# Kernel tuning notes

Hardware: AMD Instinct MI355X
Metric: run time of the kernel (lower is better)

The kernel has to match this reference:

```python
import jax, jax.numpy as jnp
import numpy as np

N_NODES = 50000
NEG_SLOPE = 0.2


def _gat_layer(x, src, dst, W, att_src, att_dst, bias, concat):
    # x: [N, F_in]; W: [F_in, H*D]; att_*: [H, D]; bias: [H*D] or [D]
    H, D = att_src.shape
    N = x.shape[0]
    h = (x @ W).reshape(N, H, D)                       # [N, H, D]
    a_s = jnp.einsum('nhd,hd->nh', h, att_src)         # [N, H]
    a_d = jnp.einsum('nhd,hd->nh', h, att_dst)
    e = a_s[src] + a_d[dst]                            # [E, H]
    e = jnp.where(e > 0, e, NEG_SLOPE * e)             # LeakyReLU(0.2)
    # segment softmax over incoming edges of each target node
    e_max = jax.ops.segment_max(e, dst, num_segments=N)
    ex = jnp.exp(e - e_max[dst])
    denom = jax.ops.segment_sum(ex, dst, num_segments=N)
    alpha = ex / denom[dst]                            # [E, H]
    msg = h[src] * alpha[:, :, None]                   # [E, H, D]
    out = jax.ops.segment_sum(msg, dst, num_segments=N)  # [N, H, D]
    if concat:
        out = out.reshape(N, H * D)
    else:
        out = out.mean(axis=1)
    return out + bias


def _forward(x, edge_index, W1, att_src1, att_dst1, b1, W2, att_src2, att_dst2, b2):
    N = x.shape[0]
    loop = jnp.arange(N, dtype=edge_index.dtype)
    src = jnp.concatenate([edge_index[0], loop])       # add self-loops (PyG default)
    dst = jnp.concatenate([edge_index[1], loop])
    h = _gat_layer(x, src, dst, W1, att_src1, att_dst1, b1, concat=True)
    h = jax.nn.elu(h)
    h = _gat_layer(h, src, dst, W2, att_src2, att_dst2, b2, concat=False)
    return jax.nn.log_softmax(h, axis=-1)


def setup_inputs() -> dict:
    key = jax.random.key(0)
    ks = jax.random.split(key, 12)
    N, E, F_in, F_out, H, D = N_NODES, 1600000, 128, 64, 8, 32
    glorot = lambda k, shp: jax.random.normal(k, shp, jnp.float32) * np.sqrt(2.0 / (shp[0] + shp[-1]))
    return {
        'x': jax.random.normal(ks[0], (N, F_in), jnp.float32),
        'edge_index': jax.random.randint(ks[1], (2, E), 0, N, jnp.int64),
        'W1': glorot(ks[2], (F_in, H * D)),
        'att_src1': glorot(ks[3], (H, D)),
        'att_dst1': glorot(ks[4], (H, D)),
        'b1': jnp.zeros((H * D,), jnp.float32),
        'W2': glorot(ks[5], (H * D, F_out)),
        'att_src2': glorot(ks[6], (1, F_out)),
        'att_dst2': glorot(ks[7], (1, F_out)),
        'b2': jnp.zeros((F_out,), jnp.float32),
    }


def reference(x, edge_index, W1, att_src1, att_dst1, b1, W2, att_src2, att_dst2, b2):
    return _forward(x, edge_index, W1, att_src1, att_dst1, b1, W2, att_src2, att_dst2, b2)
```

## Files before the change

kernel.cpp:

```cpp
#include <hip/hip_runtime.h>
#include <hip/hip_bf16.h>
#include <math.h>


#define FIN 128
#define C1 256
#define NH 8
#define HD 32
#define C2 64
#define CH1 64

typedef float floatx2 __attribute__((ext_vector_type(2)));
typedef short bf16x8 __attribute__((ext_vector_type(8)));
typedef float f32x4 __attribute__((ext_vector_type(4)));

__device__ __forceinline__ float blo(unsigned u) { return __uint_as_float(u << 16); }
__device__ __forceinline__ float bhi(unsigned u) { return __uint_as_float(u & 0xffff0000u); }
__device__ __forceinline__ unsigned pkbf(float a, float b) {
    unsigned ua = __float_as_uint(a), ub = __float_as_uint(b);
    ua += 0x7fff + ((ua >> 16) & 1);
    ub += 0x7fff + ((ub >> 16) & 1);
    return (ua >> 16) | (ub & 0xffff0000u);
}

__global__ void init_kernel(const float* __restrict__ W1, const float* __restrict__ W2,
                            int* __restrict__ cnt, unsigned short* __restrict__ w1t,
                            unsigned short* __restrict__ w2t, int n) {
    int i = blockIdx.x * 256 + threadIdx.x;
    if (i < n) cnt[i] = 1;
    if (i < C1 * FIN) {
        int j = i >> 7, k = i & 127;
        float v = W1[(size_t)k * C1 + j];
        w1t[i] = (unsigned short)(pkbf(v, v) & 0xffffu);
    } else if (i < C1 * FIN + C2 * C1) {
        int j2 = i - C1 * FIN;
        int j = j2 >> 8, k = j2 & 255;
        float v = W2[(size_t)k * C2 + j];
        w2t[j2] = (unsigned short)(pkbf(v, v) & 0xffffu);
    }
}

__global__ void hist_kernel(const int* __restrict__ ei, int E, int T,
                            int* cnt, int* __restrict__ offs) {
    int base = blockIdx.x * 256 + threadIdx.x;
    if (base >= T) return;
    int d[4], o[4];
    #pragma unroll
    for (int i = 0; i < 4; ++i) {
        int e = base + i * T;
        d[i] = (e < E) ? ei[E + e] : -1;
    }
    #pragma unroll
    for (int i = 0; i < 4; ++i)
        if (d[i] >= 0) o[i] = atomicAdd(&cnt[d[i]], 1);
    #pragma unroll
    for (int i = 0; i < 4; ++i)
        if (d[i] >= 0) offs[base + i * T] = o[i];
}

__global__ void scan1_kernel(const int* __restrict__ cnt, int n,
                             int* __restrict__ pref, int* __restrict__ bsum) {
    int tid = threadIdx.x, lane = tid & 63, w = tid >> 6;
    int i = blockIdx.x * 256 + tid;
    int v = (i < n) ? cnt[i] : 0;
    int sc = v;
    #pragma unroll
    for (int d = 1; d < 64; d <<= 1) {
        int t = __shfl_up(sc, d, 64);
        if (lane >= d) sc += t;
    }
    __shared__ int ws[4];
    if (lane == 63) ws[w] = sc;
    __syncthreads();
    int woff = 0;
    #pragma unroll
    for (int k = 0; k < 4; ++k) woff += (k < w) ? ws[k] : 0;
    if (i < n) pref[i] = woff + sc - v;
    if (tid == 255) bsum[blockIdx.x] = woff + sc;
}

__global__ void scan2_kernel(int* bsum, int nb) {
    int tid = threadIdx.x, lane = tid & 63, w = tid >> 6;
    int v = (tid < nb) ? bsum[tid] : 0;
    int sc = v;
    #pragma unroll
    for (int d = 1; d < 64; d <<= 1) {
        int t = __shfl_up(sc, d, 64);
        if (lane >= d) sc += t;
    }
    __shared__ int ws[4];
    if (lane == 63) ws[w] = sc;
    __syncthreads();
    int woff = 0;
    #pragma unroll
    for (int k = 0; k < 4; ++k) woff += (k < w) ? ws[k] : 0;
    __syncthreads();
    if (tid < nb) bsum[tid] = woff + sc - v;
}

__global__ void scan3_kernel(const int* __restrict__ pref, const int* __restrict__ bsum,
                             int n, int ETOT, int* __restrict__ rowptr,
                             int* __restrict__ colb) {
    int i = blockIdx.x * 256 + threadIdx.x;
    if (i < n) {
        int rp = pref[i] + bsum[blockIdx.x];
        rowptr[i] = rp;
        colb[rp] = i;
    }
    if (i == 0) rowptr[n] = ETOT;
}

__global__ void scatter_kernel(const int* __restrict__ ei, const int* __restrict__ rowptr,
                               const int* __restrict__ offs, int E, int T,
                               int* __restrict__ colb) {
    int base = blockIdx.x * 256 + threadIdx.x;
    if (base >= T) return;
    #pragma unroll
    for (int i = 0; i < 4; ++i) {
        int e = base + i * T;
        if (e >= E) continue;
        int src = ei[e], dst = ei[E + e];
        colb[rowptr[dst] + offs[e]] = src;
    }
}

__global__ __launch_bounds__(256) void gemm1_mfma(
    const float* __restrict__ x, const unsigned short* __restrict__ w1t,
    const float* __restrict__ att_s, const float* __restrict__ att_d,
    unsigned char* __restrict__ h1, float* __restrict__ as1, float* __restrict__ ad1, int Nn) {
    __shared__ __align__(16) unsigned char sA[64 * 256];
    int tid = threadIdx.x;
    int row0 = blockIdx.x * 64;
    #pragma unroll
    for (int rep = 0; rep < 4; ++rep) {
        int flat = rep * 256 + tid;
        int row = flat >> 4, c16 = flat & 15;
        uint4 v = make_uint4(0u, 0u, 0u, 0u);
        if (row0 + row < Nn) {
            const float4* p = reinterpret_cast<const float4*>(
                x + (size_t)(row0 + row) * FIN + c16 * 8);
            float4 f0 = p[0], f1 = p[1];
            v.x = pkbf(f0.x, f0.y); v.y = pkbf(f0.z, f0.w);
            v.z = pkbf(f1.x, f1.y); v.w = pkbf(f1.z, f1.w);
        }
        *reinterpret_cast<uint4*>(sA + ((row * 256 + c16 * 16) ^ ((row & 7) << 4))) = v;
    }
    __syncthreads();
    int w = tid >> 6, l = tid & 63;
    int lr = l & 15, lq = l >> 4;
    int arow = w * 16 + lr;
    bf16x8 a[4];
    #pragma unroll
    for (int ks = 0; ks < 4; ++ks)
        a[ks] = *reinterpret_cast<const bf16x8*>(
            sA + ((arow * 256 + ks * 64 + lq * 16) ^ ((arow & 7) << 4)));
    const unsigned char* wb = reinterpret_cast<const unsigned char*>(w1t);
    float ps[4] = {0.f, 0.f, 0.f, 0.f}, pd[4] = {0.f, 0.f, 0.f, 0.f};
    #pragma unroll
    for (int nt = 0; nt < 16; ++nt) {
        f32x4 acc = {0.f, 0.f, 0.f, 0.f};
        #pragma unroll
        for (int ks = 0; ks < 4; ++ks) {
            bf16x8 b = *reinterpret_cast<const bf16x8*>(
                wb + (size_t)(nt * 16 + lr) * 256 + ks * 64 + lq * 16);
            acc = __builtin_amdgcn_mfma_f32_16x16x32_bf16(a[ks], b, acc, 0, 0, 0);
        }
        int col = nt * 16 + lr;
        float sa = att_s[col], da = att_d[col];
        #pragma unroll
        for (int reg = 0; reg < 4; ++reg) {
            int row = row0 + w * 16 + lq * 4 + reg;
            if (row < Nn) {
                unsigned pk = __builtin_amdgcn_cvt_pk_fp8_f32(acc[reg], acc[reg], 0, false);
                h1[(size_t)row * C1 + col] = (unsigned char)(pk & 0xffu);
            }
            ps[reg] = fmaf(acc[reg], sa, ps[reg]);
            pd[reg] = fmaf(acc[reg], da, pd[reg]);
        }
        if (nt & 1) {
            #pragma unroll
            for (int reg = 0; reg < 4; ++reg) {
                #pragma unroll
                for (int mk = 8; mk >= 1; mk >>= 1) {
                    ps[reg] += __shfl_xor(ps[reg], mk, 64);
                    pd[reg] += __shfl_xor(pd[reg], mk, 64);
                }
            }
            if (lr == 0) {
                int hh = nt >> 1;
                #pragma unroll
                for (int reg = 0; reg < 4; ++reg) {
                    int row = row0 + w * 16 + lq * 4 + reg;
                    if (row < Nn) {
                        as1[row * NH + hh] = ps[reg];
                        ad1[row * NH + hh] = pd[reg];
                    }
                }
            }
            #pragma unroll
            for (int reg = 0; reg < 4; ++reg) { ps[reg] = 0.f; pd[reg] = 0.f; }
        }
    }
}

__global__ __launch_bounds__(128) void agg1_kernel(
    const int* __restrict__ rowptr, const int* __restrict__ colb,
    const float* __restrict__ as1, const float* __restrict__ ad1,
    const unsigned char* __restrict__ h1, const float* __restrict__ b1,
    __hip_bfloat16* __restrict__ x1e, int N) {
    int wid = threadIdx.x >> 6, lane = threadIdx.x & 63;
    int n = blockIdx.x * 2 + wid;
    __shared__ float sp[2][CH1 * 9];
    __shared__ int soff[2][CH1];
    __shared__ float advs[2][NH];
    if (n >= N) return;
    int start = rowptr[n], end = rowptr[n + 1];
    int h = lane >> 3, sub = lane & 7;
    int half = lane >> 5, l5 = lane & 31;
    int hq = l5 >> 2;
    soff[wid][lane] = 0;
    if (lane < NH) advs[wid][lane] = ad1[n * NH + lane];
    float adr[NH];
    #pragma unroll
    for (int hh = 0; hh < NH; ++hh) adr[hh] = advs[wid][hh];

    float m = -INFINITY, denom = 0.f;
    floatx2 A01 = {0.f, 0.f}, A23 = {0.f, 0.f}, A45 = {0.f, 0.f}, A67 = {0.f, 0.f};
    for (int base = start; base < end; base += CH1) {
        int cn = min(CH1, end - base);
        if (lane < cn) {
            int s = colb[base + lane];
            soff[wid][lane] = s << 8;
            const float4* ap = reinterpret_cast<const float4*>(as1 + (size_t)s * NH);
            float4 q0 = ap[0], q1 = ap[1];
            float av[8] = {q0.x, q0.y, q0.z, q0.w, q1.x, q1.y, q1.z, q1.w};
            #pragma unroll
            for (int hh = 0; hh < NH; ++hh) {
                float e = av[hh] + adr[hh];
                e = e > 0.f ? e : 0.2f * e;
                sp[wid][lane * 9 + hh] = e;
            }
        }
        float cmax = -INFINITY;
        for (int e = sub; e < cn; e += 8) cmax = fmaxf(cmax, sp[wid][e * 9 + h]);
        #pragma unroll
        for (int mk = 4; mk >= 1; mk >>= 1) cmax = fmaxf(cmax, __shfl_xor(cmax, mk, 64));
        float newm = fmaxf(m, cmax);
        float scale = __expf(m - newm);
        float scale_g = __shfl(scale, hq << 3, 64);
        floatx2 s2 = {scale_g, scale_g};
        A01 *= s2; A23 *= s2; A45 *= s2; A67 *= s2;
        denom *= scale; m = newm;
        float psum = 0.f;
        for (int e = sub; e < cn; e += 8) {
            float p = __expf(sp[wid][e * 9 + h] - m);
            sp[wid][e * 9 + h] = p;
            psum += p;
        }
        #pragma unroll
        for (int mk = 4; mk >= 1; mk >>= 1) psum += __shfl_xor(psum, mk, 64);
        denom += psum;
        #pragma unroll 2
        for (int e2 = 0; e2 < cn; e2 += 2) {
            int e = e2 + half;
            bool ok = e < cn;
            int off = soff[wid][ok ? e : 0];
            float p = ok ? sp[wid][e * 9 + hq] : 0.f;
            floatx2 p2 = {p, p};
            uint2 u = *reinterpret_cast<const uint2*>(h1 + off + l5 * 8);
            floatx2 f01 = __builtin_amdgcn_cvt_pk_f32_fp8((int)u.x, false);
            floatx2 f23 = __builtin_amdgcn_cvt_pk_f32_fp8((int)u.x, true);
            floatx2 f45 = __builtin_amdgcn_cvt_pk_f32_fp8((int)u.y, false);
            floatx2 f67 = __builtin_amdgcn_cvt_pk_f32_fp8((int)u.y, true);
            A01 = __builtin_elementwise_fma(p2, f01, A01);
            A23 = __builtin_elementwise_fma(p2, f23, A23);
            A45 = __builtin_elementwise_fma(p2, f45, A45);
            A67 = __builtin_elementwise_fma(p2, f67, A67);
        }
    }
    float a0 = A01.x, a1 = A01.y, a2 = A23.x, a3 = A23.y;
    float a4 = A45.x, a5 = A45.y, a6 = A67.x, a7 = A67.y;
    a0 += __shfl_xor(a0, 32, 64); a1 += __shfl_xor(a1, 32, 64);
    a2 += __shfl_xor(a2, 32, 64); a3 += __shfl_xor(a3, 32, 64);
    a4 += __shfl_xor(a4, 32, 64); a5 += __shfl_xor(a5, 32, 64);
    a6 += __shfl_xor(a6, 32, 64); a7 += __shfl_xor(a7, 32, 64);
    float invd = 1.f / __shfl(denom, hq << 3, 64);
    if (half == 0) {
        const float4* bp = reinterpret_cast<const float4*>(b1 + l5 * 8);
        float4 bv0 = bp[0], bv1 = bp[1];
        float v0 = a0 * invd + bv0.x, v1 = a1 * invd + bv0.y;
        float v2 = a2 * invd + bv0.z, v3 = a3 * invd + bv0.w;
        float v4 = a4 * invd + bv1.x, v5 = a5 * invd + bv1.y;
        float v6 = a6 * invd + bv1.z, v7 = a7 * invd + bv1.w;
        v0 = v0 > 0.f ? v0 : __expf(v0) - 1.f;
        v1 = v1 > 0.f ? v1 : __expf(v1) - 1.f;
        v2 = v2 > 0.f ? v2 : __expf(v2) - 1.f;
        v3 = v3 > 0.f ? v3 : __expf(v3) - 1.f;
        v4 = v4 > 0.f ? v4 : __expf(v4) - 1.f;
        v5 = v5 > 0.f ? v5 : __expf(v5) - 1.f;
        v6 = v6 > 0.f ? v6 : __expf(v6) - 1.f;
        v7 = v7 > 0.f ? v7 : __expf(v7) - 1.f;
        uint4 w;
        w.x = pkbf(v0, v1); w.y = pkbf(v2, v3);
        w.z = pkbf(v4, v5); w.w = pkbf(v6, v7);
        *reinterpret_cast<uint4*>(x1e + (size_t)n * C1 + l5 * 8) = w;
    }
}

__global__ __launch_bounds__(256) void gemm2_mfma(
    const unsigned short* __restrict__ x1e, const unsigned short* __restrict__ w2t,
    const float* __restrict__ att_s2, const float* __restrict__ att_d2,
    unsigned char* __restrict__ h2, float* __restrict__ as2, float* __restrict__ ad2, int Nn) {
    __shared__ __align__(16) unsigned char sA[64 * 512];
    int tid = threadIdx.x;
    int row0 = blockIdx.x * 64;
    #pragma unroll
    for (int rep = 0; rep < 8; ++rep) {
        int flat = rep * 256 + tid;
        int row = flat >> 5, c16 = flat & 31;
        uint4 v = make_uint4(0u, 0u, 0u, 0u);
        if (row0 + row < Nn)
            v = *reinterpret_cast<const uint4*>(
                reinterpret_cast<const unsigned char*>(x1e) + (size_t)(row0 + row) * 512 + c16 * 16);
        *reinterpret_cast<uint4*>(sA + ((row * 512 + c16 * 16) ^ ((row & 7) << 4))) = v;
    }
    __syncthreads();
    int w = tid >> 6, l = tid & 63;
    int lr = l & 15, lq = l >> 4;
    int arow = w * 16 + lr;
    bf16x8 a[8];
    #pragma unroll
    for (int ks = 0; ks < 8; ++ks)
        a[ks] = *reinterpret_cast<const bf16x8*>(
            sA + ((arow * 512 + ks * 64 + lq * 16) ^ ((arow & 7) << 4)));
    const unsigned char* wb = reinterpret_cast<const unsigned char*>(w2t);
    float ps[4] = {0.f, 0.f, 0.f, 0.f}, pd[4] = {0.f, 0.f, 0.f, 0.f};
    #pragma unroll
    for (int nt = 0; nt < 4; ++nt) {
        f32x4 acc = {0.f, 0.f, 0.f, 0.f};
        #pragma unroll
        for (int ks = 0; ks < 8; ++ks) {
            bf16x8 b = *reinterpret_cast<const bf16x8*>(
                wb + (size_t)(nt * 16 + lr) * 512 + ks * 64 + lq * 16);
            acc = __builtin_amdgcn_mfma_f32_16x16x32_bf16(a[ks], b, acc, 0, 0, 0);
        }
        int col = nt * 16 + lr;
        float sa = att_s2[col], da = att_d2[col];
        #pragma unroll
        for (int reg = 0; reg < 4; ++reg) {
            int row = row0 + w * 16 + lq * 4 + reg;
            if (row < Nn) {
                unsigned pk = __builtin_amdgcn_cvt_pk_fp8_f32(acc[reg], acc[reg], 0, false);
                h2[(size_t)row * C2 + col] = (unsigned char)(pk & 0xffu);
            }
            ps[reg] = fmaf(acc[reg], sa, ps[reg]);
            pd[reg] = fmaf(acc[reg], da, pd[reg]);
        }
    }
    #pragma unroll
    for (int reg = 0; reg < 4; ++reg) {
        #pragma unroll
        for (int mk = 8; mk >= 1; mk >>= 1) {
            ps[reg] += __shfl_xor(ps[reg], mk, 64);
            pd[reg] += __shfl_xor(pd[reg], mk, 64);
        }
    }
    if (lr == 0) {
        #pragma unroll
        for (int reg = 0; reg < 4; ++reg) {
            int row = row0 + w * 16 + lq * 4 + reg;
            if (row < Nn) { as2[row] = ps[reg]; ad2[row] = pd[reg]; }
        }
    }
}

__global__ __launch_bounds__(128) void agg2_kernel(
    const int* __restrict__ rowptr, const int* __restrict__ colb,
    const float* __restrict__ as2, const float* __restrict__ ad2,
    const unsigned char* __restrict__ h2, const float* __restrict__ b2,
    float* __restrict__ out, int N) {
    int wid = threadIdx.x >> 6, lane = threadIdx.x & 63;
    int n = blockIdx.x * 2 + wid;
    __shared__ float sp2[2][64];
    __shared__ int soff2[2][64];
    if (n >= N) return;
    int start = rowptr[n], end = rowptr[n + 1];
    int q = lane >> 4, l4 = lane & 15;
    soff2[wid][lane] = 0;
    float adn = ad2[n];
    float m = -INFINITY, denom = 0.f;
    floatx2 A01 = {0.f, 0.f}, A23 = {0.f, 0.f};
    for (int base = start; base < end; base += 64) {
        int cn = min(64, end - base);
        float logit = -INFINITY;
        if (lane < cn) {
            int s = colb[base + lane];
            soff2[wid][lane] = s << 6;
            float e = as2[s] + adn;
            logit = e > 0.f ? e : 0.2f * e;
        }
        float cmax = logit;
        #pragma unroll
        for (int mk = 32; mk >= 1; mk >>= 1) cmax = fmaxf(cmax, __shfl_xor(cmax, mk, 64));
        float newm = fmaxf(m, cmax);
        float scale = __expf(m - newm);
        floatx2 s2 = {scale, scale};
        A01 *= s2; A23 *= s2;
        denom *= scale; m = newm;
        float p = (lane < cn) ? __expf(logit - m) : 0.f;
        sp2[wid][lane] = p;
        float psum = p;
        #pragma unroll
        for (int mk = 32; mk >= 1; mk >>= 1) psum += __shfl_xor(psum, mk, 64);
        denom += psum;
        #pragma unroll 2
        for (int e2 = 0; e2 < cn; e2 += 4) {
            int e = e2 + q;
            bool ok = e < cn;
            int off = soff2[wid][ok ? e : 0];
            float pe = ok ? sp2[wid][e] : 0.f;
            floatx2 p2 = {pe, pe};
            unsigned u = *reinterpret_cast<const unsigned*>(h2 + off + l4 * 4);
            floatx2 f01 = __builtin_amdgcn_cvt_pk_f32_fp8((int)u, false);
            floatx2 f23 = __builtin_amdgcn_cvt_pk_f32_fp8((int)u, true);
            A01 = __builtin_elementwise_fma(p2, f01, A01);
            A23 = __builtin_elementwise_fma(p2, f23, A23);
        }
    }
    float a0 = A01.x, a1 = A01.y, a2 = A23.x, a3 = A23.y;
    a0 += __shfl_xor(a0, 16, 64); a1 += __shfl_xor(a1, 16, 64);
    a2 += __shfl_xor(a2, 16, 64); a3 += __shfl_xor(a3, 16, 64);
    a0 += __shfl_xor(a0, 32, 64); a1 += __shfl_xor(a1, 32, 64);
    a2 += __shfl_xor(a2, 32, 64); a3 += __shfl_xor(a3, 32, 64);
    float invd = 1.f / denom;
    const float4* bp = reinterpret_cast<const float4*>(b2 + l4 * 4);
    float4 bv = bp[0];
    float v0 = a0 * invd + bv.x, v1 = a1 * invd + bv.y;
    float v2 = a2 * invd + bv.z, v3 = a3 * invd + bv.w;
    float mx = fmaxf(fmaxf(v0, v1), fmaxf(v2, v3));
    #pragma unroll
    for (int mk = 8; mk >= 1; mk >>= 1) mx = fmaxf(mx, __shfl_xor(mx, mk, 64));
    float sum = __expf(v0 - mx) + __expf(v1 - mx) + __expf(v2 - mx) + __expf(v3 - mx);
    #pragma unroll
    for (int mk = 8; mk >= 1; mk >>= 1) sum += __shfl_xor(sum, mk, 64);
    float ls = logf(sum);
    if (q == 0) {
        float4 o = make_float4(v0 - mx - ls, v1 - mx - ls, v2 - mx - ls, v3 - mx - ls);
        *reinterpret_cast<float4*>(out + (size_t)n * C2 + l4 * 4) = o;
    }
}

extern "C" void kernel_launch(void* const* d_in, const int* in_sizes, int n_in,
                              void* d_out, int out_size, void* d_ws, size_t ws_size,
                              hipStream_t stream) {
    const float* x      = (const float*)d_in[0];
    const int*   ei     = (const int*)d_in[1];
    const float* W1     = (const float*)d_in[2];
    const float* att_s1 = (const float*)d_in[3];
    const float* att_d1 = (const float*)d_in[4];
    const float* b1     = (const float*)d_in[5];
    const float* W2     = (const float*)d_in[6];
    const float* att_s2 = (const float*)d_in[7];
    const float* att_d2 = (const float*)d_in[8];
    const float* b2     = (const float*)d_in[9];
    float* out = (float*)d_out;

    const int N = out_size / C2;
    const int E = in_sizes[1] / 2;
    const int ETOT = E + N;
    const int NB = (N + 255) / 256;

    char* ws = (char*)d_ws;
    size_t off = 0;
    auto alloc = [&](size_t bytes) -> void* {
        void* p = ws + off;
        off += (bytes + 255) & ~(size_t)255;
        return p;
    };
    unsigned char* h1 = (unsigned char*)alloc((size_t)N * C1);
    __hip_bfloat16* x1e = (__hip_bfloat16*)alloc((size_t)N * C1 * 2);
    unsigned short* w1t = (unsigned short*)alloc((size_t)C1 * FIN * 2);
    unsigned short* w2t = (unsigned short*)alloc((size_t)C2 * C1 * 2);
    float* as1  = (float*)alloc((size_t)N * NH * 4);
    float* ad1  = (float*)alloc((size_t)N * NH * 4);
    float* as2  = (float*)alloc((size_t)N * 4);
    float* ad2  = (float*)alloc((size_t)N * 4);
    int*   cnt    = (int*)alloc((size_t)N * 4);
    int*   rowptr = (int*)alloc((size_t)(N + 1) * 4);
    int*   pref   = (int*)alloc((size_t)N * 4);
    int*   bsum   = (int*)alloc((size_t)NB * 4);
    int*   offs   = (int*)alloc((size_t)E * 4);
    int*   colb   = (int*)alloc((size_t)ETOT * 4);
    unsigned char* h2 = h1;

    const int T = (E + 3) / 4;
    init_kernel<<<(N + 255) / 256, 256, 0, stream>>>(W1, W2, cnt, w1t, w2t, N);
    hist_kernel<<<(T + 255) / 256, 256, 0, stream>>>(ei, E, T, cnt, offs);
    scan1_kernel<<<NB, 256, 0, stream>>>(cnt, N, pref, bsum);
    scan2_kernel<<<1, 256, 0, stream>>>(bsum, NB);
    scan3_kernel<<<NB, 256, 0, stream>>>(pref, bsum, N, ETOT, rowptr, colb);
    scatter_kernel<<<(T + 255) / 256, 256, 0, stream>>>(ei, rowptr, offs, E, T, colb);

    gemm1_mfma<<<(N + 63) / 64, 256, 0, stream>>>(x, w1t, att_s1, att_d1, h1, as1, ad1, N);
    agg1_kernel<<<(N + 1) / 2, 128, 0, stream>>>(rowptr, colb, as1, ad1, h1, b1, x1e, N);

    gemm2_mfma<<<(N + 63) / 64, 256, 0, stream>>>((const unsigned short*)x1e, w2t,
                                                  att_s2, att_d2, h2, as2, ad2, N);
    agg2_kernel<<<(N + 1) / 2, 128, 0, stream>>>(rowptr, colb, as2, ad2, h2, b2, out, N);
}
```

Baseline: 275.7 us.

## Merge CSR scatter into gemm1 launch and use one-wave blocks for aggregation

The CSR scatter kernel is folded into the gemm1 launch as extra blocks, so the two independent workloads can run concurrently and one launch and its serialization point are removed. Both aggregation kernels now launch one 64-thread block per node instead of two waves per block, which shrinks per-block shared memory and removes the early-exit handling of a partial block. This trades more, smaller blocks (more scheduling overhead) for finer-grained load balancing across nodes of varying degree.

```diff
diff --git a/kernel.cpp b/kernel.cpp
--- a/kernel.cpp
+++ b/kernel.cpp
@@ -110,26 +110,27 @@
     if (i == 0) rowptr[n] = ETOT;
 }
 
-__global__ void scatter_kernel(const int* __restrict__ ei, const int* __restrict__ rowptr,
-                               const int* __restrict__ offs, int E, int T,
-                               int* __restrict__ colb) {
-    int base = blockIdx.x * 256 + threadIdx.x;
-    if (base >= T) return;
-    #pragma unroll
-    for (int i = 0; i < 4; ++i) {
-        int e = base + i * T;
-        if (e >= E) continue;
-        int src = ei[e], dst = ei[E + e];
-        colb[rowptr[dst] + offs[e]] = src;
-    }
-}
-
-__global__ __launch_bounds__(256) void gemm1_mfma(
+__global__ __launch_bounds__(256) void gemm1_scatter_fused(
     const float* __restrict__ x, const unsigned short* __restrict__ w1t,
     const float* __restrict__ att_s, const float* __restrict__ att_d,
-    unsigned char* __restrict__ h1, float* __restrict__ as1, float* __restrict__ ad1, int Nn) {
+    unsigned char* __restrict__ h1, float* __restrict__ as1, float* __restrict__ ad1,
+    int Nn, int GB1,
+    const int* __restrict__ ei, const int* __restrict__ rowptr,
+    const int* __restrict__ offs, int E, int T, int* __restrict__ colb) {
     __shared__ __align__(16) unsigned char sA[64 * 256];
     int tid = threadIdx.x;
+    if (blockIdx.x >= GB1) {
+        int base = (blockIdx.x - GB1) * 256 + tid;
+        if (base >= T) return;
+        #pragma unroll
+        for (int i = 0; i < 4; ++i) {
+            int e = base + i * T;
+            if (e >= E) continue;
+            int src = ei[e], dst = ei[E + e];
+            colb[rowptr[dst] + offs[e]] = src;
+        }
+        return;
+    }
     int row0 = blockIdx.x * 64;
     #pragma unroll
     for (int rep = 0; rep < 4; ++rep) {
@@ -203,26 +204,25 @@
     }
 }
 
-__global__ __launch_bounds__(128) void agg1_kernel(
+__global__ __launch_bounds__(64) void agg1_kernel(
     const int* __restrict__ rowptr, const int* __restrict__ colb,
     const float* __restrict__ as1, const float* __restrict__ ad1,
     const unsigned char* __restrict__ h1, const float* __restrict__ b1,
     __hip_bfloat16* __restrict__ x1e, int N) {
-    int wid = threadIdx.x >> 6, lane = threadIdx.x & 63;
-    int n = blockIdx.x * 2 + wid;
-    __shared__ float sp[2][CH1 * 9];
-    __shared__ int soff[2][CH1];
-    __shared__ float advs[2][NH];
-    if (n >= N) return;
+    int lane = threadIdx.x;
+    int n = blockIdx.x;
+    __shared__ float sp[CH1 * 9];
+    __shared__ int soff[CH1];
+    __shared__ float advs[NH];
     int start = rowptr[n], end = rowptr[n + 1];
     int h = lane >> 3, sub = lane & 7;
     int half = lane >> 5, l5 = lane & 31;
     int hq = l5 >> 2;
-    soff[wid][lane] = 0;
-    if (lane < NH) advs[wid][lane] = ad1[n * NH + lane];
+    soff[lane] = 0;
+    if (lane < NH) advs[lane] = ad1[n * NH + lane];
     float adr[NH];
     #pragma unroll
-    for (int hh = 0; hh < NH; ++hh) adr[hh] = advs[wid][hh];
+    for (int hh = 0; hh < NH; ++hh) adr[hh] = advs[hh];
 
     float m = -INFINITY, denom = 0.f;
     floatx2 A01 = {0.f, 0.f}, A23 = {0.f, 0.f}, A45 = {0.f, 0.f}, A67 = {0.f, 0.f};
@@ -230,7 +230,7 @@
         int cn = min(CH1, end - base);
         if (lane < cn) {
             int s = colb[base + lane];
-            soff[wid][lane] = s << 8;
+            soff[lane] = s << 8;
             const float4* ap = reinterpret_cast<const float4*>(as1 + (size_t)s * NH);
             float4 q0 = ap[0], q1 = ap[1];
             float av[8] = {q0.x, q0.y, q0.z, q0.w, q1.x, q1.y, q1.z, q1.w};
@@ -238,11 +238,11 @@
             for (int hh = 0; hh < NH; ++hh) {
                 float e = av[hh] + adr[hh];
                 e = e > 0.f ? e : 0.2f * e;
-                sp[wid][lane * 9 + hh] = e;
+                sp[lane * 9 + hh] = e;
             }
         }
         float cmax = -INFINITY;
-        for (int e = sub; e < cn; e += 8) cmax = fmaxf(cmax, sp[wid][e * 9 + h]);
+        for (int e = sub; e < cn; e += 8) cmax = fmaxf(cmax, sp[e * 9 + h]);
         #pragma unroll
         for (int mk = 4; mk >= 1; mk >>= 1) cmax = fmaxf(cmax, __shfl_xor(cmax, mk, 64));
         float newm = fmaxf(m, cmax);
@@ -253,8 +253,8 @@
         denom *= scale; m = newm;
         float psum = 0.f;
         for (int e = sub; e < cn; e += 8) {
-            float p = __expf(sp[wid][e * 9 + h] - m);
-            sp[wid][e * 9 + h] = p;
+            float p = __expf(sp[e * 9 + h] - m);
+            sp[e * 9 + h] = p;
             psum += p;
         }
         #pragma unroll
@@ -264,8 +264,8 @@
         for (int e2 = 0; e2 < cn; e2 += 2) {
             int e = e2 + half;
             bool ok = e < cn;
-            int off = soff[wid][ok ? e : 0];
-            float p = ok ? sp[wid][e * 9 + hq] : 0.f;
+            int off = soff[ok ? e : 0];
+            float p = ok ? sp[e * 9 + hq] : 0.f;
             floatx2 p2 = {p, p};
             uint2 u = *reinterpret_cast<const uint2*>(h1 + off + l5 * 8);
             floatx2 f01 = __builtin_amdgcn_cvt_pk_f32_fp8((int)u.x, false);
@@ -374,19 +374,18 @@
     }
 }
 
-__global__ __launch_bounds__(128) void agg2_kernel(
+__global__ __launch_bounds__(64) void agg2_kernel(
     const int* __restrict__ rowptr, const int* __restrict__ colb,
     const float* __restrict__ as2, const float* __restrict__ ad2,
     const unsigned char* __restrict__ h2, const float* __restrict__ b2,
     float* __restrict__ out, int N) {
-    int wid = threadIdx.x >> 6, lane = threadIdx.x & 63;
-    int n = blockIdx.x * 2 + wid;
-    __shared__ float sp2[2][64];
-    __shared__ int soff2[2][64];
-    if (n >= N) return;
+    int lane = threadIdx.x;
+    int n = blockIdx.x;
+    __shared__ float sp2[64];
+    __shared__ int soff2[64];
     int start = rowptr[n], end = rowptr[n + 1];
     int q = lane >> 4, l4 = lane & 15;
-    soff2[wid][lane] = 0;
+    soff2[lane] = 0;
     float adn = ad2[n];
     float m = -INFINITY, denom = 0.f;
     floatx2 A01 = {0.f, 0.f}, A23 = {0.f, 0.f};
@@ -395,7 +394,7 @@
         float logit = -INFINITY;
         if (lane < cn) {
             int s = colb[base + lane];
-            soff2[wid][lane] = s << 6;
+            soff2[lane] = s << 6;
             float e = as2[s] + adn;
             logit = e > 0.f ? e : 0.2f * e;
         }
@@ -408,7 +407,7 @@
         A01 *= s2; A23 *= s2;
         denom *= scale; m = newm;
         float p = (lane < cn) ? __expf(logit - m) : 0.f;
-        sp2[wid][lane] = p;
+        sp2[lane] = p;
         float psum = p;
         #pragma unroll
         for (int mk = 32; mk >= 1; mk >>= 1) psum += __shfl_xor(psum, mk, 64);
@@ -417,8 +416,8 @@
         for (int e2 = 0; e2 < cn; e2 += 4) {
             int e = e2 + q;
             bool ok = e < cn;
-            int off = soff2[wid][ok ? e : 0];
-            float pe = ok ? sp2[wid][e] : 0.f;
+            int off = soff2[ok ? e : 0];
+            float pe = ok ? sp2[e] : 0.f;
             floatx2 p2 = {pe, pe};
             unsigned u = *reinterpret_cast<const unsigned*>(h2 + off + l4 * 4);
             floatx2 f01 = __builtin_amdgcn_cvt_pk_f32_fp8((int)u, false);
@@ -499,12 +498,15 @@
     scan1_kernel<<<NB, 256, 0, stream>>>(cnt, N, pref, bsum);
     scan2_kernel<<<1, 256, 0, stream>>>(bsum, NB);
     scan3_kernel<<<NB, 256, 0, stream>>>(pref, bsum, N, ETOT, rowptr, colb);
-    scatter_kernel<<<(T + 255) / 256, 256, 0, stream>>>(ei, rowptr, offs, E, T, colb);
-
-    gemm1_mfma<<<(N + 63) / 64, 256, 0, stream>>>(x, w1t, att_s1, att_d1, h1, as1, ad1, N);
-    agg1_kernel<<<(N + 1) / 2, 128, 0, stream>>>(rowptr, colb, as1, ad1, h1, b1, x1e, N);
+
+    const int GB1 = (N + 63) / 64;
+    const int GSC = (T + 255) / 256;
+    gemm1_scatter_fused<<<GB1 + GSC, 256, 0, stream>>>(
+        x, w1t, att_s1, att_d1, h1, as1, ad1, N, GB1, ei, rowptr, offs, E, T, colb);
+
+    agg1_kernel<<<N, 64, 0, stream>>>(rowptr, colb, as1, ad1, h1, b1, x1e, N);
 
     gemm2_mfma<<<(N + 63) / 64, 256, 0, stream>>>((const unsigned short*)x1e, w2t,
                                                   att_s2, att_d2, h2, as2, ad2, N);
-    agg2_kernel<<<(N + 1) / 2, 128, 0, stream>>>(rowptr, colb, as2, ad2, h2, b2, out, N);
-}
+    agg2_kernel<<<N, 64, 0, stream>>>(rowptr, colb, as2, ad2, h2, b2, out, N);
+}
```

After: 258.3 us. 1.07x faster.
